# Performance work log

Hardware: AMD Instinct MI355X
Metric: run time of the kernel (lower is better)

Reference implementation:

```python
import jax, jax.numpy as jnp
import numpy as np

BITS = 4
NIBBLES_PER_INT32 = 8  # 32 // 4
K, N, GROUP = 4096, 4096, 128
TOKENS = 8192


def setup_inputs() -> dict:
    key = jax.random.key(0)
    kx, kw, kz, ks = jax.random.split(key, 4)
    x = jax.random.normal(kx, (TOKENS, K), dtype=jnp.float32)
    # packed 4-bit weights: 8 nibbles per int32 word along the K axis
    qweight = jax.random.randint(kw, (K // NIBBLES_PER_INT32, N), jnp.iinfo(jnp.int32).min, jnp.iinfo(jnp.int32).max, dtype=jnp.int32)
    # packed 4-bit zero points: 8 nibbles per int32 word along the N axis
    G = K // GROUP
    qzeros = jax.random.randint(kz, (G, N // NIBBLES_PER_INT32), jnp.iinfo(jnp.int32).min, jnp.iinfo(jnp.int32).max, dtype=jnp.int32)
    # per-group scales (positive)
    scales = jax.random.uniform(ks, (G, N), dtype=jnp.float32, minval=0.001, maxval=0.02)
    g_idx = (jnp.arange(K, dtype=jnp.int32) // GROUP).astype(jnp.int32)
    return {"x": x, "qweight": qweight, "qzeros": qzeros, "scales": scales, "g_idx": g_idx}


def _unpack_rows(packed):
    # packed: [K//8, N] int32 -> [K, N] int32 nibbles (packed along rows)
    shifts = jnp.arange(NIBBLES_PER_INT32, dtype=jnp.int32) * BITS  # [8]
    nib = (packed[:, None, :] >> shifts[None, :, None]) & 0xF       # [K//8, 8, N]
    return nib.reshape(-1, packed.shape[1])                          # [K, N]


def _unpack_cols(packed):
    # packed: [G, N//8] int32 -> [G, N] int32 nibbles (packed along cols)
    shifts = jnp.arange(NIBBLES_PER_INT32, dtype=jnp.int32) * BITS  # [8]
    nib = (packed[:, :, None] >> shifts[None, None, :]) & 0xF       # [G, N//8, 8]
    return nib.reshape(packed.shape[0], -1)                          # [G, N]


def reference(x, qweight, qzeros, scales, g_idx):
    # GPTQ-style dequant: W[k, n] = (int_w[k, n] - z[g_idx[k], n]) * s[g_idx[k], n]
    w_int = _unpack_rows(qweight)                 # [K, N] in [0, 15]
    z_int = _unpack_cols(qzeros)                  # [G, N] in [0, 15]
    z = z_int[g_idx]                              # [K, N]
    s = scales[g_idx]                             # [K, N]
    W = (w_int - z).astype(scales.dtype) * s      # [K, N] dequantized
    return x @ W                                  # [TOKENS, N]
```

## Files before the change

kernel.cpp:

```cpp
#include <hip/hip_runtime.h>
#include <stdint.h>

#define M_DIM 8192
#define K_DIM 4096
#define N_DIM 4096

typedef int   i32x4 __attribute__((ext_vector_type(4)));
typedef float f32x4 __attribute__((ext_vector_type(4)));

__device__ __forceinline__ void gload16(const void* g, void* l) {
    __builtin_amdgcn_global_load_lds(
        (const __attribute__((address_space(1))) void*)g,
        (__attribute__((address_space(3))) void*)l,
        16, 0, 0);
}

__global__ __launch_bounds__(256) void conv_x_i8(const float* __restrict__ x,
                                                 int* __restrict__ xq,
                                                 float* __restrict__ xs) {
    int m = blockIdx.x, tid = threadIdx.x;
    const float* row = x + (size_t)m * K_DIM;
    float4 v[4];
    float mx = 0.f;
    #pragma unroll
    for (int i = 0; i < 4; ++i) {
        v[i] = *(const float4*)(row + i * 1024 + tid * 4);
        mx = fmaxf(mx, fmaxf(fmaxf(fabsf(v[i].x), fabsf(v[i].y)),
                             fmaxf(fabsf(v[i].z), fabsf(v[i].w))));
    }
    #pragma unroll
    for (int o = 32; o > 0; o >>= 1) mx = fmaxf(mx, __shfl_xor(mx, o, 64));
    __shared__ float red[4];
    if ((tid & 63) == 0) red[tid >> 6] = mx;
    __syncthreads();
    mx = fmaxf(fmaxf(red[0], red[1]), fmaxf(red[2], red[3]));
    mx = fmaxf(mx, 1e-20f);
    float inv = 127.f / mx;
    if (tid == 0) xs[m] = mx * (1.f / 127.f);
    #pragma unroll
    for (int i = 0; i < 4; ++i) {
        int q0 = (int)__builtin_rintf(v[i].x * inv);
        int q1 = (int)__builtin_rintf(v[i].y * inv);
        int q2 = (int)__builtin_rintf(v[i].z * inv);
        int q3 = (int)__builtin_rintf(v[i].w * inv);
        uint32_t p = (uint32_t)(q0 & 255) | ((uint32_t)(q1 & 255) << 8) |
                     ((uint32_t)(q2 & 255) << 16) | ((uint32_t)q3 << 24);
        xq[(size_t)m * (K_DIM / 4) + i * 256 + tid] = (int)p;
    }
}

#define DLROW 272
__global__ __launch_bounds__(256) void dequant_i8(const uint32_t* __restrict__ qw,
                                                  const uint32_t* __restrict__ qz,
                                                  const int* __restrict__ gidx,
                                                  signed char* __restrict__ wt) {
    __shared__ __align__(16) unsigned char lds[64 * DLROW];
    int tid = threadIdx.x;
    int n0  = blockIdx.x * 64;
    int k80 = blockIdx.y * 32;

    #pragma unroll
    for (int i = 0; i < 8; ++i) {
        int idx = i * 256 + tid;
        int k8l = idx >> 6;
        int nl  = idx & 63;
        int k8  = k80 + k8l;
        int nn  = n0 + nl;
        uint32_t w = qw[(size_t)k8 * N_DIM + nn];
        int g = gidx[k8 * 8];
        uint32_t zw = qz[(size_t)g * (N_DIM / 8) + (nn >> 3)];
        int z = (int)((zw >> ((nn & 7) * 4)) & 0xFu);
        uint64_t o = 0;
        #pragma unroll
        for (int j = 0; j < 8; ++j) {
            int wv = (int)((w >> (4 * j)) & 0xFu);
            o |= (uint64_t)(uint8_t)(signed char)(wv - z) << (8 * j);
        }
        *(uint64_t*)&lds[nl * DLROW + k8l * 8] = o;
    }
    __syncthreads();
    #pragma unroll
    for (int i = 0; i < 4; ++i) {
        int idx = i * 256 + tid;
        int row = idx >> 4;
        int c   = idx & 15;
        i32x4 v = *(const i32x4*)&lds[row * DLROW + c * 16];
        *(i32x4*)&wt[(size_t)(n0 + row) * K_DIM + k80 * 8 + c * 16] = v;
    }
}

#define VMW(n) asm volatile("s_waitcnt vmcnt(" #n ")" ::: "memory")

#define STAGE_A(bufi, t, s, j)                                                   \
    gload16(ga + ((size_t)((s) * 32 + (j) * 128) * K_DIM + (size_t)(t) * 128),   \
            &As[bufi][((((s) * 32 + (j) * 128 + brl)) << 7) + sc * 16])

#define STAGE_B(bufi, t, s)                                                      \
    gload16(gb + ((size_t)((s) * 32) * K_DIM + (size_t)(t) * 128),               \
            &Bs[bufi][((((s) * 32 + brl)) << 7) + sc * 16])

#define STAGE_S(p, t)                                                            \
    gload16(S + (size_t)((t) + (lane >> 5)) * N_DIM + bn + (lane & 31) * 4,      \
            &Sl[p][lane * 4])

#define PHASE(bufi, p, mq, nq, STG, TAIL) do {                                   \
    i32x4 af_[2][2], bf_[2][2];                                                  \
    float sv0_ = Sl[p][(bufi) * 128 + wave_n * 64 + (nq) * 32 + l15];            \
    float sv1_ = Sl[p][(bufi) * 128 + wave_n * 64 + (nq) * 32 + 16 + l15];       \
    _Pragma("unroll")                                                            \
    for (int m2_ = 0; m2_ < 2; ++m2_) {                                          \
        const signed char* p_ =                                                  \
            &As[bufi][(wave_m * 64 + ((mq) * 2 + m2_) * 16 + l15) << 7];         \
        af_[m2_][0] = *(const i32x4*)(p_ + c0);                                  \
        af_[m2_][1] = *(const i32x4*)(p_ + c1);                                  \
    }                                                                            \
    _Pragma("unroll")                                                            \
    for (int n2_ = 0; n2_ < 2; ++n2_) {                                          \
        const signed char* p_ =                                                  \
            &Bs[bufi][(wave_n * 64 + ((nq) * 2 + n2_) * 16 + l15) << 7];         \
        bf_[n2_][0] = *(const i32x4*)(p_ + c0);                                  \
        bf_[n2_][1] = *(const i32x4*)(p_ + c1);                                  \
    }                                                                            \
    STG;                                                                         \
    __builtin_amdgcn_s_barrier();                                                \
    asm volatile("s_waitcnt lgkmcnt(0)" ::: "memory");                           \
    __builtin_amdgcn_s_setprio(1);                                               \
    _Pragma("unroll")                                                            \
    for (int m2_ = 0; m2_ < 2; ++m2_) {                                          \
        _Pragma("unroll")                                                        \
        for (int n2_ = 0; n2_ < 2; ++n2_) {                                      \
            i32x4 t0_ = __builtin_amdgcn_mfma_i32_16x16x64_i8(                   \
                af_[m2_][0], bf_[n2_][0], (i32x4){0, 0, 0, 0}, 0, 0, 0);         \
            i32x4 t1_ = __builtin_amdgcn_mfma_i32_16x16x64_i8(                   \
                af_[m2_][1], bf_[n2_][1], t0_, 0, 0, 0);                         \
            float ss_ = (n2_ ? sv1_ : sv0_);                                     \
            _Pragma("unroll")                                                    \
            for (int r_ = 0; r_ < 4; ++r_)                                       \
                facc[(mq) * 2 + m2_][(nq) * 2 + n2_][r_] += (float)t1_[r_] * ss_;\
        }                                                                        \
    }                                                                            \
    __builtin_amdgcn_s_setprio(0);                                               \
    TAIL;                                                                        \
    __builtin_amdgcn_s_barrier();                                                \
    __builtin_amdgcn_sched_barrier(0);                                           \
} while (0)

__global__ __launch_bounds__(512, 2) void gemm_i8(const signed char* __restrict__ A,
                                                  const signed char* __restrict__ B,
                                                  const float* __restrict__ S,
                                                  const float* __restrict__ XS,
                                                  float* __restrict__ C) {
    __shared__ __align__(16) signed char As[2][256 * 128];
    __shared__ __align__(16) signed char Bs[2][128 * 128];
    __shared__ __align__(16) float Sl[2][256];

    const int tid  = threadIdx.x;
    const int lane = tid & 63;
    const int wid  = tid >> 6;
    const int l15  = lane & 15;
    const int quad = lane >> 4;
    const int wave_m = wid >> 1;
    const int wave_n = wid & 1;
    const int h  = l15 & 7;
    const int c0 = (quad ^ h) * 16;
    const int c1 = ((4 + quad) ^ h) * 16;

    int bid = blockIdx.x;
    int swz = (bid & 7) * 128 + (bid >> 3);
    int bm = (swz >> 5) * 256;
    int bn = (swz & 31) * 128;

    const int sr  = tid >> 3;
    const int sc  = tid & 7;
    const int gch = sc ^ (sr & 7);
    const int brl = (sr & 31) + ((sr >> 5) << 6);
    const signed char* ga = A + (size_t)(bm + brl) * K_DIM + gch * 16;
    const signed char* gb = B + (size_t)(bn + brl) * K_DIM + gch * 16;

    f32x4 facc[4][4];
    #pragma unroll
    for (int i = 0; i < 4; ++i)
        #pragma unroll
        for (int j = 0; j < 4; ++j)
            facc[i][j] = (f32x4){0.f, 0.f, 0.f, 0.f};

    STAGE_S(0, 0);
    STAGE_A(0, 0, 0, 0); STAGE_A(0, 0, 0, 1);
    STAGE_B(0, 0, 0);
    STAGE_A(0, 0, 1, 0); STAGE_A(0, 0, 1, 1);
    STAGE_B(0, 0, 1);
    STAGE_A(1, 1, 0, 0); STAGE_A(1, 1, 0, 1);
    STAGE_B(1, 1, 0);
    VMW(6);
    __builtin_amdgcn_s_barrier();
    __builtin_amdgcn_sched_barrier(0);

    #pragma clang loop unroll(disable)
    for (int it = 0; it < 16; ++it) {
        const int t0k = 2 * it;
        const int t1k = 2 * it + 1;
        const bool nl = (it < 15);
        const int p = it & 1;

        PHASE(0, p, 0, 0,
              { if (nl) { STAGE_S(p ^ 1, t0k + 2); }
                STAGE_A(1, t1k, 1, 0); STAGE_A(1, t1k, 1, 1); },
              { if (nl) { VMW(6); } else { VMW(5); } });
        PHASE(0, p, 0, 1,
              { STAGE_B(1, t1k, 1); },
              {});
        PHASE(0, p, 1, 0,
              { if (nl) { STAGE_A(0, t0k + 2, 0, 0); STAGE_A(0, t0k + 2, 0, 1); } },
              {});
        PHASE(0, p, 1, 1,
              { if (nl) { STAGE_B(0, t0k + 2, 0); } },
              { if (nl) { VMW(7); } else { VMW(3); } });
        PHASE(1, p, 0, 0,
              { if (nl) { STAGE_A(0, t0k + 2, 1, 0); STAGE_A(0, t0k + 2, 1, 1); } },
              { if (nl) { VMW(5); } else { VMW(0); } });
        PHASE(1, p, 0, 1,
              { if (nl) { STAGE_B(0, t0k + 2, 1); } },
              {});
        PHASE(1, p, 1, 0,
              { if (nl) { STAGE_A(1, t1k + 2, 0, 0); STAGE_A(1, t1k + 2, 0, 1); } },
              {});
        PHASE(1, p, 1, 1,
              { if (nl) { STAGE_B(1, t1k + 2, 0); } },
              { if (nl) { VMW(6); } });
    }

    #pragma unroll
    for (int mt = 0; mt < 4; ++mt) {
        int row0 = bm + wave_m * 64 + mt * 16 + quad * 4;
        float4 xsv = *(const float4*)(XS + row0);
        #pragma unroll
        for (int nt = 0; nt < 4; ++nt) {
            int col = bn + wave_n * 64 + nt * 16 + l15;
            C[(size_t)(row0 + 0) * N_DIM + col] = facc[mt][nt][0] * xsv.x;
            C[(size_t)(row0 + 1) * N_DIM + col] = facc[mt][nt][1] * xsv.y;
            C[(size_t)(row0 + 2) * N_DIM + col] = facc[mt][nt][2] * xsv.z;
            C[(size_t)(row0 + 3) * N_DIM + col] = facc[mt][nt][3] * xsv.w;
        }
    }
}

extern "C" void kernel_launch(void* const* d_in, const int* in_sizes, int n_in,
                              void* d_out, int out_size, void* d_ws, size_t ws_size,
                              hipStream_t stream) {
    const float*    x    = (const float*)d_in[0];
    const uint32_t* qw   = (const uint32_t*)d_in[1];
    const uint32_t* qz   = (const uint32_t*)d_in[2];
    const float*    sc   = (const float*)d_in[3];
    const int*      gidx = (const int*)d_in[4];
    float* out = (float*)d_out;

    signed char* xq = (signed char*)d_ws;
    signed char* wt = xq + (size_t)M_DIM * K_DIM;
    float*       xs = (float*)(wt + (size_t)N_DIM * K_DIM);

    conv_x_i8<<<dim3(M_DIM), 256, 0, stream>>>(x, (int*)xq, xs);
    dequant_i8<<<dim3(N_DIM / 64, K_DIM / 256), 256, 0, stream>>>(qw, qz, gidx, wt);
    gemm_i8<<<dim3(1024), dim3(512), 0, stream>>>(xq, wt, sc, xs, out);
}
```

Measured before the change: 475.3 us.

## Restructure int8 GEMM phases to software-pipeline group rescale behind MFMAs

Each k-step is reorganised from 8 phases of 2x2 MFMA tiles into 4 phases of 4x2 tiles. The A fragments now stay in registers across the two n-halves, and the int32 MFMA results are double-buffered so the float rescale of the previous phase runs after the current phase's MFMAs are issued. The global-to-LDS staging order and the vmcnt waits are rescheduled to match, and occupancy is now set through amdgpu_waves_per_eu instead of the launch-bounds minimum. This is meant to cut LDS re-reads and hide the dependent-convert latency, at the cost of higher register pressure and a riskier wait-count schedule.

Result: slower. 537.4 us (+13.1%).

```diff
diff --git a/kernel.cpp b/kernel.cpp
--- a/kernel.cpp
+++ b/kernel.cpp
@@ -99,57 +99,71 @@
     gload16(gb + ((size_t)((s) * 32) * K_DIM + (size_t)(t) * 128),               \
             &Bs[bufi][((((s) * 32 + brl)) << 7) + sc * 16])
 
-#define STAGE_S(p, t)                                                            \
+#define STAGE_S(slot, t)                                                         \
     gload16(S + (size_t)((t) + (lane >> 5)) * N_DIM + bn + (lane & 31) * 4,      \
-            &Sl[p][lane * 4])
-
-#define PHASE(bufi, p, mq, nq, STG, TAIL) do {                                   \
-    i32x4 af_[2][2], bf_[2][2];                                                  \
-    float sv0_ = Sl[p][(bufi) * 128 + wave_n * 64 + (nq) * 32 + l15];            \
-    float sv1_ = Sl[p][(bufi) * 128 + wave_n * 64 + (nq) * 32 + 16 + l15];       \
+            &Sl[slot][lane * 4])
+
+#define RESC(iacS, svS, snq)                                                     \
     _Pragma("unroll")                                                            \
-    for (int m2_ = 0; m2_ < 2; ++m2_) {                                          \
-        const signed char* p_ =                                                  \
-            &As[bufi][(wave_m * 64 + ((mq) * 2 + m2_) * 16 + l15) << 7];         \
-        af_[m2_][0] = *(const i32x4*)(p_ + c0);                                  \
-        af_[m2_][1] = *(const i32x4*)(p_ + c1);                                  \
+    for (int mt_ = 0; mt_ < 4; ++mt_) {                                          \
+        _Pragma("unroll")                                                        \
+        for (int n2_ = 0; n2_ < 2; ++n2_) {                                      \
+            float ss_ = svS[(snq) * 2 + n2_];                                    \
+            _Pragma("unroll")                                                    \
+            for (int r_ = 0; r_ < 4; ++r_)                                       \
+                facc[mt_][(snq) * 2 + n2_][r_] +=                                \
+                    (float)iacS[mt_][n2_][r_] * ss_;                             \
+        }                                                                        \
+    }
+
+#define PHASE(bufi, nq, TSTART, svN, iacW, iacR, svR, snq, STG, TAIL) do {       \
+    if (TSTART) {                                                                \
+        _Pragma("unroll")                                                        \
+        for (int nt_ = 0; nt_ < 4; ++nt_)                                        \
+            svN[nt_] = Sl[pp][(bufi) * 128 + wave_n * 64 + nt_ * 16 + l15];      \
+        _Pragma("unroll")                                                        \
+        for (int mt_ = 0; mt_ < 4; ++mt_) {                                      \
+            const signed char* p_ =                                              \
+                &As[bufi][(wave_m * 64 + mt_ * 16 + l15) << 7];                  \
+            afr[mt_][0] = *(const i32x4*)(p_ + c0);                              \
+            afr[mt_][1] = *(const i32x4*)(p_ + c1);                              \
+        }                                                                        \
     }                                                                            \
     _Pragma("unroll")                                                            \
     for (int n2_ = 0; n2_ < 2; ++n2_) {                                          \
         const signed char* p_ =                                                  \
             &Bs[bufi][(wave_n * 64 + ((nq) * 2 + n2_) * 16 + l15) << 7];         \
-        bf_[n2_][0] = *(const i32x4*)(p_ + c0);                                  \
-        bf_[n2_][1] = *(const i32x4*)(p_ + c1);                                  \
+        bfr[n2_][0] = *(const i32x4*)(p_ + c0);                                  \
+        bfr[n2_][1] = *(const i32x4*)(p_ + c1);                                  \
     }                                                                            \
     STG;                                                                         \
     __builtin_amdgcn_s_barrier();                                                \
     asm volatile("s_waitcnt lgkmcnt(0)" ::: "memory");                           \
     __builtin_amdgcn_s_setprio(1);                                               \
     _Pragma("unroll")                                                            \
-    for (int m2_ = 0; m2_ < 2; ++m2_) {                                          \
+    for (int mt_ = 0; mt_ < 4; ++mt_) {                                          \
         _Pragma("unroll")                                                        \
         for (int n2_ = 0; n2_ < 2; ++n2_) {                                      \
             i32x4 t0_ = __builtin_amdgcn_mfma_i32_16x16x64_i8(                   \
-                af_[m2_][0], bf_[n2_][0], (i32x4){0, 0, 0, 0}, 0, 0, 0);         \
-            i32x4 t1_ = __builtin_amdgcn_mfma_i32_16x16x64_i8(                   \
-                af_[m2_][1], bf_[n2_][1], t0_, 0, 0, 0);                         \
-            float ss_ = (n2_ ? sv1_ : sv0_);                                     \
-            _Pragma("unroll")                                                    \
-            for (int r_ = 0; r_ < 4; ++r_)                                       \
-                facc[(mq) * 2 + m2_][(nq) * 2 + n2_][r_] += (float)t1_[r_] * ss_;\
+                afr[mt_][0], bfr[n2_][0], (i32x4){0, 0, 0, 0}, 0, 0, 0);         \
+            iacW[mt_][n2_] = __builtin_amdgcn_mfma_i32_16x16x64_i8(              \
+                afr[mt_][1], bfr[n2_][1], t0_, 0, 0, 0);                         \
         }                                                                        \
     }                                                                            \
+    RESC(iacR, svR, snq);                                                        \
     __builtin_amdgcn_s_setprio(0);                                               \
     TAIL;                                                                        \
     __builtin_amdgcn_s_barrier();                                                \
     __builtin_amdgcn_sched_barrier(0);                                           \
 } while (0)
 
-__global__ __launch_bounds__(512, 2) void gemm_i8(const signed char* __restrict__ A,
-                                                  const signed char* __restrict__ B,
-                                                  const float* __restrict__ S,
-                                                  const float* __restrict__ XS,
-                                                  float* __restrict__ C) {
+__global__ __launch_bounds__(512)
+__attribute__((amdgpu_waves_per_eu(2, 2)))
+void gemm_i8(const signed char* __restrict__ A,
+             const signed char* __restrict__ B,
+             const float* __restrict__ S,
+             const float* __restrict__ XS,
+             float* __restrict__ C) {
     __shared__ __align__(16) signed char As[2][256 * 128];
     __shared__ __align__(16) signed char Bs[2][128 * 128];
     __shared__ __align__(16) float Sl[2][256];
@@ -178,56 +192,55 @@
     const signed char* gb = B + (size_t)(bn + brl) * K_DIM + gch * 16;
 
     f32x4 facc[4][4];
-    #pragma unroll
-    for (int i = 0; i < 4; ++i)
+    i32x4 afr[4][2], bfr[2][2];
+    i32x4 iax[4][2], iay[4][2];
+    float sva[4], svb[4];
+    #pragma unroll
+    for (int i = 0; i < 4; ++i) {
         #pragma unroll
         for (int j = 0; j < 4; ++j)
             facc[i][j] = (f32x4){0.f, 0.f, 0.f, 0.f};
+        iay[i][0] = (i32x4){0, 0, 0, 0};
+        iay[i][1] = (i32x4){0, 0, 0, 0};
+    }
+    svb[0] = svb[1] = svb[2] = svb[3] = 0.f;
 
     STAGE_S(0, 0);
+    STAGE_B(0, 0, 0);
+    STAGE_B(0, 0, 1);
     STAGE_A(0, 0, 0, 0); STAGE_A(0, 0, 0, 1);
-    STAGE_B(0, 0, 0);
     STAGE_A(0, 0, 1, 0); STAGE_A(0, 0, 1, 1);
-    STAGE_B(0, 0, 1);
-    STAGE_A(1, 1, 0, 0); STAGE_A(1, 1, 0, 1);
     STAGE_B(1, 1, 0);
-    VMW(6);
+    VMW(1);
     __builtin_amdgcn_s_barrier();
     __builtin_amdgcn_sched_barrier(0);
 
     #pragma clang loop unroll(disable)
     for (int it = 0; it < 16; ++it) {
+        const int pp  = it & 1;
         const int t0k = 2 * it;
         const int t1k = 2 * it + 1;
         const bool nl = (it < 15);
-        const int p = it & 1;
-
-        PHASE(0, p, 0, 0,
-              { if (nl) { STAGE_S(p ^ 1, t0k + 2); }
+
+        PHASE(0, 0, 1, sva, iax, iay, svb, 1,
+              { if (nl) { STAGE_S(pp ^ 1, t0k + 2); }
+                STAGE_B(1, t1k, 1);
+                STAGE_A(1, t1k, 0, 0); STAGE_A(1, t1k, 0, 1);
                 STAGE_A(1, t1k, 1, 0); STAGE_A(1, t1k, 1, 1); },
-              { if (nl) { VMW(6); } else { VMW(5); } });
-        PHASE(0, p, 0, 1,
-              { STAGE_B(1, t1k, 1); },
               {});
-        PHASE(0, p, 1, 0,
-              { if (nl) { STAGE_A(0, t0k + 2, 0, 0); STAGE_A(0, t0k + 2, 0, 1); } },
+        PHASE(0, 1, 0, sva, iay, iax, sva, 0,
+              { if (nl) { STAGE_B(0, t0k + 2, 0); } },
+              { if (nl) { VMW(1); } else { VMW(0); } });
+        PHASE(1, 0, 1, svb, iax, iay, sva, 1,
+              { if (nl) { STAGE_B(0, t0k + 2, 1);
+                          STAGE_A(0, t0k + 2, 0, 0); STAGE_A(0, t0k + 2, 0, 1);
+                          STAGE_A(0, t0k + 2, 1, 0); STAGE_A(0, t0k + 2, 1, 1); } },
               {});
-        PHASE(0, p, 1, 1,
-              { if (nl) { STAGE_B(0, t0k + 2, 0); } },
-              { if (nl) { VMW(7); } else { VMW(3); } });
-        PHASE(1, p, 0, 0,
-              { if (nl) { STAGE_A(0, t0k + 2, 1, 0); STAGE_A(0, t0k + 2, 1, 1); } },
-              { if (nl) { VMW(5); } else { VMW(0); } });
-        PHASE(1, p, 0, 1,
-              { if (nl) { STAGE_B(0, t0k + 2, 1); } },
-              {});
-        PHASE(1, p, 1, 0,
-              { if (nl) { STAGE_A(1, t1k + 2, 0, 0); STAGE_A(1, t1k + 2, 0, 1); } },
-              {});
-        PHASE(1, p, 1, 1,
+        PHASE(1, 1, 0, svb, iay, iax, svb, 0,
               { if (nl) { STAGE_B(1, t1k + 2, 0); } },
-              { if (nl) { VMW(6); } });
-    }
+              { if (nl) { VMW(1); } });
+    }
+    RESC(iay, svb, 1);
 
     #pragma unroll
     for (int mt = 0; mt < 4; ++mt) {
```
